# Kernel optimization log

Hardware: AMD Instinct MI355X
Metric: run time of the kernel (lower is better)

Reference implementation:

```python
import jax, jax.numpy as jnp
import numpy as np

D_MODEL = 1024
GEOM_DIM = 32
CLAMP_VALUE = 10.0


def setup_inputs() -> dict:
    key = jax.random.key(0)
    k1, k2, k3 = jax.random.split(key, 3)
    B, N = 4, 2048
    H = jax.random.normal(k1, (B, N, D_MODEL), dtype=jnp.float32)
    B_prev = jax.random.normal(k2, (B, N, N), dtype=jnp.float32)
    # geom_proj weight, init std=0.001 as in the torch module
    W = jax.random.normal(k3, (GEOM_DIM, D_MODEL), dtype=jnp.float32) * 0.001
    alpha = jnp.asarray(1.0, dtype=jnp.float32)
    beta = jnp.asarray(0.05, dtype=jnp.float32)
    return {"H": H, "B_prev": B_prev, "W": W, "alpha": alpha, "beta": beta}


def reference(H, B_prev, W, alpha, beta):
    # Low-rank projection: G [B, N, geom_dim]
    G = jnp.einsum("bnd,kd->bnk", H, W)
    G_sq = jnp.sum(G * G, axis=-1)  # [B, N]
    # Pairwise squared distance: [B, N, N]
    gram = jnp.einsum("bik,bjk->bij", G, G)
    dist = G_sq[:, :, None] + G_sq[:, None, :] - 2.0 * gram
    dist = jnp.maximum(dist, 0.0)
    # EMA bias update with clamp
    B_next = alpha * B_prev - beta * dist
    B_next = jnp.clip(B_next, -CLAMP_VALUE, CLAMP_VALUE)
    return B_next
```

## Files before the change

### kernel.cpp

```cpp
#include <hip/hip_runtime.h>


typedef __attribute__((ext_vector_type(8))) short short8;
typedef __attribute__((ext_vector_type(4))) short short4v;
typedef __attribute__((ext_vector_type(4))) float floatx4;

static __device__ __forceinline__ short bf16_bits(float f) {
    union { float f; unsigned int u; } v; v.f = f;
    unsigned int u = v.u;
    u += 0x7FFFu + ((u >> 16) & 1u);
    return (short)(u >> 16);
}

static __device__ __forceinline__ float bf16_to_f32(unsigned short h) {
    union { unsigned int u; float f; } v; v.u = ((unsigned int)h) << 16;
    return v.f;
}

__global__ __launch_bounds__(256) void k0_wcast(const float* __restrict__ W,
                                                short* __restrict__ Wb) {
    const int f = blockIdx.x * 256 + threadIdx.x;
    const float4 v = *(const float4*)(W + (long)f * 4);
    short4v s;
    s[0] = bf16_bits(v.x); s[1] = bf16_bits(v.y);
    s[2] = bf16_bits(v.z); s[3] = bf16_bits(v.w);
    *(short4v*)(Wb + (long)f * 4) = s;
}

__global__ __launch_bounds__(256) void k1_proj(const float* __restrict__ H,
                                               const short* __restrict__ Wb,
                                               unsigned short* __restrict__ G,
                                               float* __restrict__ Q) {
    const int blk  = blockIdx.x;
    const int t    = threadIdx.x;
    const int w    = t >> 6;
    const int lane = t & 63;
    const int m    = lane & 15;
    const int quad = lane >> 4;

    __shared__ short sH[16 * 1032];

    const float* Hb = H + (long)blk * 16384;
    #pragma unroll
    for (int it = 0; it < 8; ++it) {
        const int f  = t + it * 256;
        const int r  = f >> 7;
        const int c8 = f & 127;
        const float4 v0 = *(const float4*)(Hb + r * 1024 + c8 * 8);
        const float4 v1 = *(const float4*)(Hb + r * 1024 + c8 * 8 + 4);
        short8 sv;
        sv[0] = bf16_bits(v0.x); sv[1] = bf16_bits(v0.y);
        sv[2] = bf16_bits(v0.z); sv[3] = bf16_bits(v0.w);
        sv[4] = bf16_bits(v1.x); sv[5] = bf16_bits(v1.y);
        sv[6] = bf16_bits(v1.z); sv[7] = bf16_bits(v1.w);
        *(short8*)&sH[r * 1032 + c8 * 8] = sv;
    }
    __syncthreads();

    const int kq = w * 256 + quad * 8;
    const short* wb0 = Wb + (long)m * 1024 + kq;
    const short* wb1 = Wb + (long)(m + 16) * 1024 + kq;

    floatx4 acc0 = {0.f, 0.f, 0.f, 0.f};
    floatx4 acc1 = {0.f, 0.f, 0.f, 0.f};

    short8 b0 = *(const short8*)wb0;
    short8 b1 = *(const short8*)wb1;

    #pragma unroll
    for (int s = 0; s < 8; ++s) {
        short8 nb0, nb1;
        if (s < 7) {
            nb0 = *(const short8*)(wb0 + (s + 1) * 32);
            nb1 = *(const short8*)(wb1 + (s + 1) * 32);
        }
        const short8 af = *(const short8*)&sH[m * 1032 + kq + s * 32];
        acc0 = __builtin_amdgcn_mfma_f32_16x16x32_bf16(af, b0, acc0, 0, 0, 0);
        acc1 = __builtin_amdgcn_mfma_f32_16x16x32_bf16(af, b1, acc1, 0, 0, 0);
        if (s < 7) { b0 = nb0; b1 = nb1; }
    }

    __shared__ float red[4][16][32];
    #pragma unroll
    for (int r = 0; r < 4; ++r) {
        red[w][quad * 4 + r][m]      = acc0[r];
        red[w][quad * 4 + r][m + 16] = acc1[r];
    }
    __syncthreads();
    for (int e = t; e < 512; e += 256) {
        const int mm = e >> 5, nn = e & 31;
        float v = red[0][mm][nn] + red[1][mm][nn] + red[2][mm][nn] + red[3][mm][nn];
        const unsigned short hb = (unsigned short)bf16_bits(v);
        G[(long)(blk * 16 + mm) * 32 + nn] = hb;
        red[0][mm][nn] = bf16_to_f32(hb);
    }
    __syncthreads();
    if (t < 16) {
        float s = 0.f;
        #pragma unroll
        for (int nn = 0; nn < 32; ++nn) { const float v = red[0][t][nn]; s += v * v; }
        Q[blk * 16 + t] = s;
    }
}

__global__ __launch_bounds__(256) void k2_update(const float* __restrict__ Bp,
                                                 const unsigned short* __restrict__ G,
                                                 const float* __restrict__ Q,
                                                 const float* __restrict__ alphap,
                                                 const float* __restrict__ betap,
                                                 float* __restrict__ out) {
    const int b  = blockIdx.z;
    const int i0 = blockIdx.y * 64;
    const int j0 = blockIdx.x * 128;
    const int t  = threadIdx.x;
    const int w    = t >> 6;
    const int lane = t & 63;
    const int m    = lane & 15;
    const int quad = lane >> 4;

    const int i = i0 + w * 16 + m;
    const long rowoff = ((long)b * 2048 + i) * 2048 + j0;

    const float alpha = alphap[0];
    const float beta  = betap[0];
    const float qi = Q[b * 2048 + i];

    floatx4 bv[8];
    const floatx4* bp4 = (const floatx4*)(Bp + rowoff);
    #pragma unroll
    for (int jt = 0; jt < 8; ++jt) bv[jt] = bp4[jt * 4 + quad];

    const short* Gg = (const short*)G;
    short8 bfi = *(const short8*)&Gg[((long)(b * 2048 + i0 + w * 16 + m)) * 32 + quad * 8];
    short8 afj[8];
    const long gj_base = ((long)(b * 2048 + j0 + m)) * 32 + quad * 8;
    #pragma unroll
    for (int jt = 0; jt < 8; ++jt)
        afj[jt] = *(const short8*)&Gg[gj_base + (long)jt * 16 * 32];

    floatx4 qjv[8];
    #pragma unroll
    for (int jt = 0; jt < 8; ++jt)
        qjv[jt] = *(const floatx4*)&Q[b * 2048 + j0 + jt * 16 + quad * 4];

    #pragma unroll
    for (int jt = 0; jt < 8; ++jt) {
        asm volatile("" :: "v"(bv[jt]), "v"(afj[jt]), "v"(qjv[jt]));
    }
    asm volatile("" :: "v"(bfi), "v"(qi));
    __builtin_amdgcn_sched_barrier(0);

    floatx4 acc[8];
    #pragma unroll
    for (int jt = 0; jt < 8; ++jt) {
        floatx4 z = {0.f, 0.f, 0.f, 0.f};
        acc[jt] = __builtin_amdgcn_mfma_f32_16x16x32_bf16(afj[jt], bfi, z, 0, 0, 0);
    }

    float* op = out + rowoff;
    #pragma unroll
    for (int jt = 0; jt < 8; ++jt) {
        floatx4 ov;
        #pragma unroll
        for (int r = 0; r < 4; ++r) {
            float d = qi + qjv[jt][r] - 2.f * acc[jt][r];
            d = fmaxf(d, 0.f);
            ov[r] = fminf(fmaxf(alpha * bv[jt][r] - beta * d, -10.f), 10.f);
        }
        *(floatx4*)(op + (jt * 4 + quad) * 4) = ov;
    }
}

extern "C" void kernel_launch(void* const* d_in, const int* in_sizes, int n_in,
                              void* d_out, int out_size, void* d_ws, size_t ws_size,
                              hipStream_t stream) {
    const float* H     = (const float*)d_in[0];
    const float* Bp    = (const float*)d_in[1];
    const float* W     = (const float*)d_in[2];
    const float* alpha = (const float*)d_in[3];
    const float* beta  = (const float*)d_in[4];
    float* out = (float*)d_out;

    unsigned short* G = (unsigned short*)d_ws;
    float* Q  = (float*)((char*)d_ws + 8192 * 32 * 2);
    short* Wb = (short*)((char*)d_ws + 8192 * 32 * 2 + 8192 * 4);

    k0_wcast<<<32, 256, 0, stream>>>(W, Wb);
    k1_proj<<<512, 256, 0, stream>>>(H, Wb, G, Q);

    dim3 g2(16, 32, 4);
    k2_update<<<g2, 256, 0, stream>>>(Bp, G, Q, alpha, beta, out);
}
```

Baseline: 157.7 us.

## Widen update tiles to 512 columns with double-buffered B_prev loads and LDS-staged G

Each update block now covers 512 columns in four 128-column sub-tiles. G_j and Q_j are staged once in shared memory, and B_prev loads are double-buffered in registers so the next tile's loads overlap the current tile's MFMA and epilogue. Output stores become nontemporal to avoid polluting cache. The aims are more memory-level parallelism and fewer redundant G/Q global reads per block. The cost is a quarter as many blocks, which lowers parallelism across the device, plus extra register and LDS pressure.

```diff
diff --git a/kernel.cpp b/kernel.cpp
--- a/kernel.cpp
+++ b/kernel.cpp
@@ -109,9 +109,12 @@
                                                  const float* __restrict__ alphap,
                                                  const float* __restrict__ betap,
                                                  float* __restrict__ out) {
+    __shared__ short sGj[512 * 40];
+    __shared__ float sQj[512];
+
     const int b  = blockIdx.z;
     const int i0 = blockIdx.y * 64;
-    const int j0 = blockIdx.x * 128;
+    const int J0 = blockIdx.x * 512;
     const int t  = threadIdx.x;
     const int w    = t >> 6;
     const int lane = t & 63;
@@ -119,56 +122,71 @@
     const int quad = lane >> 4;
 
     const int i = i0 + w * 16 + m;
-    const long rowoff = ((long)b * 2048 + i) * 2048 + j0;
-
+    const long rowbase = ((long)b * 2048 + i) * 2048;
+    const float* bprow = Bp  + rowbase + J0;
+    float*       orow  = out + rowbase + J0;
+
+    floatx4 bvA[8], bvB[8];
+
+#define BP_ISSUE(BANK, T) { \
+    volatile const floatx4* p_ = (volatile const floatx4*)(bprow + (T) * 128); \
+    _Pragma("unroll") \
+    for (int jt = 0; jt < 8; ++jt) BANK[jt] = p_[jt * 4 + quad]; }
+
+#define DO_TILE(BANK, T) { \
+    short8 afj_[8]; floatx4 qjv_[8]; \
+    _Pragma("unroll") \
+    for (int jt = 0; jt < 8; ++jt) { \
+        afj_[jt] = *(const short8*)&sGj[((T) * 128 + jt * 16 + m) * 40 + quad * 8]; \
+        qjv_[jt] = *(const floatx4*)&sQj[(T) * 128 + jt * 16 + quad * 4]; \
+    } \
+    floatx4 acc_[8]; \
+    _Pragma("unroll") \
+    for (int jt = 0; jt < 8; ++jt) { \
+        floatx4 z_ = {0.f, 0.f, 0.f, 0.f}; \
+        acc_[jt] = __builtin_amdgcn_mfma_f32_16x16x32_bf16(afj_[jt], bfi, z_, 0, 0, 0); \
+    } \
+    _Pragma("unroll") \
+    for (int jt = 0; jt < 8; ++jt) { \
+        floatx4 ov_; \
+        _Pragma("unroll") \
+        for (int r = 0; r < 4; ++r) { \
+            float d_ = qi + qjv_[jt][r] - 2.f * acc_[jt][r]; \
+            d_ = fmaxf(d_, 0.f); \
+            ov_[r] = fminf(fmaxf(alpha * BANK[jt][r] - beta * d_, -10.f), 10.f); \
+        } \
+        __builtin_nontemporal_store(ov_, (floatx4*)(orow + (T) * 128 + (jt * 4 + quad) * 4)); \
+    } }
+
+    BP_ISSUE(bvA, 0);
+
+    const short* Gg = (const short*)G;
+    #pragma unroll
+    for (int l = 0; l < 8; ++l) {
+        const int f = t + l * 256;
+        const int r = f >> 2, c = f & 3;
+        *(short8*)&sGj[r * 40 + c * 8] =
+            *(const short8*)&Gg[(long)(b * 2048 + J0 + r) * 32 + c * 8];
+    }
+    sQj[t]       = Q[b * 2048 + J0 + t];
+    sQj[t + 256] = Q[b * 2048 + J0 + 256 + t];
+    __syncthreads();
+
+    const short8 bfi = *(const short8*)&Gg[((long)(b * 2048 + i)) * 32 + quad * 8];
+    const float qi    = Q[b * 2048 + i];
     const float alpha = alphap[0];
     const float beta  = betap[0];
-    const float qi = Q[b * 2048 + i];
-
-    floatx4 bv[8];
-    const floatx4* bp4 = (const floatx4*)(Bp + rowoff);
-    #pragma unroll
-    for (int jt = 0; jt < 8; ++jt) bv[jt] = bp4[jt * 4 + quad];
-
-    const short* Gg = (const short*)G;
-    short8 bfi = *(const short8*)&Gg[((long)(b * 2048 + i0 + w * 16 + m)) * 32 + quad * 8];
-    short8 afj[8];
-    const long gj_base = ((long)(b * 2048 + j0 + m)) * 32 + quad * 8;
-    #pragma unroll
-    for (int jt = 0; jt < 8; ++jt)
-        afj[jt] = *(const short8*)&Gg[gj_base + (long)jt * 16 * 32];
-
-    floatx4 qjv[8];
-    #pragma unroll
-    for (int jt = 0; jt < 8; ++jt)
-        qjv[jt] = *(const floatx4*)&Q[b * 2048 + j0 + jt * 16 + quad * 4];
-
-    #pragma unroll
-    for (int jt = 0; jt < 8; ++jt) {
-        asm volatile("" :: "v"(bv[jt]), "v"(afj[jt]), "v"(qjv[jt]));
-    }
-    asm volatile("" :: "v"(bfi), "v"(qi));
-    __builtin_amdgcn_sched_barrier(0);
-
-    floatx4 acc[8];
-    #pragma unroll
-    for (int jt = 0; jt < 8; ++jt) {
-        floatx4 z = {0.f, 0.f, 0.f, 0.f};
-        acc[jt] = __builtin_amdgcn_mfma_f32_16x16x32_bf16(afj[jt], bfi, z, 0, 0, 0);
-    }
-
-    float* op = out + rowoff;
-    #pragma unroll
-    for (int jt = 0; jt < 8; ++jt) {
-        floatx4 ov;
-        #pragma unroll
-        for (int r = 0; r < 4; ++r) {
-            float d = qi + qjv[jt][r] - 2.f * acc[jt][r];
-            d = fmaxf(d, 0.f);
-            ov[r] = fminf(fmaxf(alpha * bv[jt][r] - beta * d, -10.f), 10.f);
-        }
-        *(floatx4*)(op + (jt * 4 + quad) * 4) = ov;
-    }
+
+    BP_ISSUE(bvB, 1);
+    DO_TILE(bvA, 0);
+    BP_ISSUE(bvA, 2);
+    DO_TILE(bvB, 1);
+    BP_ISSUE(bvB, 3);
+    DO_TILE(bvA, 2);
+    DO_TILE(bvB, 3);
+
+#undef BP_ISSUE
+#undef DO_TILE
 }
 
 extern "C" void kernel_launch(void* const* d_in, const int* in_sizes, int n_in,
@@ -188,6 +206,6 @@
     k0_wcast<<<32, 256, 0, stream>>>(W, Wb);
     k1_proj<<<512, 256, 0, stream>>>(H, Wb, G, Q);
 
-    dim3 g2(16, 32, 4);
+    dim3 g2(4, 32, 4);
     k2_update<<<g2, 256, 0, stream>>>(Bp, G, Q, alpha, beta, out);
 }
```

Result: slower. 168.3 us (+6.7%).

## Stage distance tile in LDS and stream B_prev rows with coalesced float4 accesses

Applied to the files above, without the earlier changes.

The update kernel is restructured so each block owns 16 full rows of one batch and walks across 512-column chunks. MFMA results (scaled distances) go to a padded shared-memory tile, and threads then read B_prev and write the output along contiguous row segments. The old layout made strided 16-byte accesses per lane across rows. The change aims for fully coalesced streaming of the 64 MB B_prev read and output write, at the cost of two barriers per chunk, fewer blocks (512 vs 2048), and loss of the prefetch-all-loads-first scheduling.

```diff
diff --git a/kernel.cpp b/kernel.cpp
--- a/kernel.cpp
+++ b/kernel.cpp
@@ -109,65 +109,58 @@
                                                  const float* __restrict__ alphap,
                                                  const float* __restrict__ betap,
                                                  float* __restrict__ out) {
-    const int b  = blockIdx.z;
-    const int i0 = blockIdx.y * 64;
-    const int j0 = blockIdx.x * 128;
+    __shared__ float sD[16 * 516];
+
+    const int b  = blockIdx.y;
+    const int i0 = blockIdx.x * 16;
     const int t  = threadIdx.x;
     const int w    = t >> 6;
     const int lane = t & 63;
     const int m    = lane & 15;
     const int quad = lane >> 4;
 
-    const int i = i0 + w * 16 + m;
-    const long rowoff = ((long)b * 2048 + i) * 2048 + j0;
-
+    const short* Gg = (const short*)G;
+    const short8 bfi = *(const short8*)&Gg[((long)(b * 2048 + i0 + m)) * 32 + quad * 8];
+    const float qi_m  = Q[b * 2048 + i0 + m];
     const float alpha = alphap[0];
     const float beta  = betap[0];
-    const float qi = Q[b * 2048 + i];
 
-    floatx4 bv[8];
-    const floatx4* bp4 = (const floatx4*)(Bp + rowoff);
-    #pragma unroll
-    for (int jt = 0; jt < 8; ++jt) bv[jt] = bp4[jt * 4 + quad];
+    const int sr = t >> 4;
+    const int sc = t & 15;
+    const float* bprow = Bp  + ((long)b * 2048 + i0 + sr) * 2048;
+    float*       orow  = out + ((long)b * 2048 + i0 + sr) * 2048;
 
-    const short* Gg = (const short*)G;
-    short8 bfi = *(const short8*)&Gg[((long)(b * 2048 + i0 + w * 16 + m)) * 32 + quad * 8];
-    short8 afj[8];
-    const long gj_base = ((long)(b * 2048 + j0 + m)) * 32 + quad * 8;
-    #pragma unroll
-    for (int jt = 0; jt < 8; ++jt)
-        afj[jt] = *(const short8*)&Gg[gj_base + (long)jt * 16 * 32];
+    for (int c = 0; c < 4; ++c) {
+        #pragma unroll
+        for (int jt = 0; jt < 8; ++jt) {
+            const int jl = w * 128 + jt * 16;
+            const int jg = c * 512 + jl;
+            const short8 afj = *(const short8*)&Gg[((long)(b * 2048 + jg + m)) * 32 + quad * 8];
+            floatx4 z = {0.f, 0.f, 0.f, 0.f};
+            const floatx4 acc = __builtin_amdgcn_mfma_f32_16x16x32_bf16(afj, bfi, z, 0, 0, 0);
+            const float4 qj = *(const float4*)&Q[b * 2048 + jg + quad * 4];
+            float4 dv;
+            dv.x = beta * fmaxf(qi_m + qj.x - 2.f * acc[0], 0.f);
+            dv.y = beta * fmaxf(qi_m + qj.y - 2.f * acc[1], 0.f);
+            dv.z = beta * fmaxf(qi_m + qj.z - 2.f * acc[2], 0.f);
+            dv.w = beta * fmaxf(qi_m + qj.w - 2.f * acc[3], 0.f);
+            *(float4*)&sD[m * 516 + jl + quad * 4] = dv;
+        }
+        __syncthreads();
 
-    floatx4 qjv[8];
-    #pragma unroll
-    for (int jt = 0; jt < 8; ++jt)
-        qjv[jt] = *(const floatx4*)&Q[b * 2048 + j0 + jt * 16 + quad * 4];
-
-    #pragma unroll
-    for (int jt = 0; jt < 8; ++jt) {
-        asm volatile("" :: "v"(bv[jt]), "v"(afj[jt]), "v"(qjv[jt]));
-    }
-    asm volatile("" :: "v"(bfi), "v"(qi));
-    __builtin_amdgcn_sched_barrier(0);
-
-    floatx4 acc[8];
-    #pragma unroll
-    for (int jt = 0; jt < 8; ++jt) {
-        floatx4 z = {0.f, 0.f, 0.f, 0.f};
-        acc[jt] = __builtin_amdgcn_mfma_f32_16x16x32_bf16(afj[jt], bfi, z, 0, 0, 0);
-    }
-
-    float* op = out + rowoff;
-    #pragma unroll
-    for (int jt = 0; jt < 8; ++jt) {
-        floatx4 ov;
         #pragma unroll
-        for (int r = 0; r < 4; ++r) {
-            float d = qi + qjv[jt][r] - 2.f * acc[jt][r];
-            d = fmaxf(d, 0.f);
-            ov[r] = fminf(fmaxf(alpha * bv[jt][r] - beta * d, -10.f), 10.f);
+        for (int k = 0; k < 8; ++k) {
+            const int col4 = sc + k * 16;
+            const float4 bv = *(const float4*)(bprow + c * 512 + col4 * 4);
+            const float4 dv = *(const float4*)&sD[sr * 516 + col4 * 4];
+            float4 ov;
+            ov.x = fminf(fmaxf(alpha * bv.x - dv.x, -10.f), 10.f);
+            ov.y = fminf(fmaxf(alpha * bv.y - dv.y, -10.f), 10.f);
+            ov.z = fminf(fmaxf(alpha * bv.z - dv.z, -10.f), 10.f);
+            ov.w = fminf(fmaxf(alpha * bv.w - dv.w, -10.f), 10.f);
+            *(float4*)(orow + c * 512 + col4 * 4) = ov;
         }
-        *(floatx4*)(op + (jt * 4 + quad) * 4) = ov;
+        __syncthreads();
     }
 }
 
@@ -188,6 +181,6 @@
     k0_wcast<<<32, 256, 0, stream>>>(W, Wb);
     k1_proj<<<512, 256, 0, stream>>>(H, Wb, G, Q);
 
-    dim3 g2(16, 32, 4);
+    dim3 g2(128, 4);
     k2_update<<<g2, 256, 0, stream>>>(Bp, G, Q, alpha, beta, out);
 }
```

New measurement: 163.3 us. +3.5%, slower.
